# Performance work log

Hardware: AMD Instinct MI355X
Metric: run time of the kernel (lower is better)

The kernel has to match this reference:

```python
import jax, jax.numpy as jnp
import numpy as np

N, C, K, H = 100000, 128, 16, 128
MIX_IN = 2 * C + 1 + C   # x, mean_feat, boundary_score, coord_embed
GATE_IN = 2 * C + 1


def _mlp2(x, w1, b1, w2, b2):
    # Linear -> GELU(exact) -> Linear (dropout=0 at eval)
    return jax.nn.gelu(x @ w1 + b1, approximate=False) @ w2 + b2


def setup_inputs() -> dict:
    key = jax.random.key(0)
    ks = jax.random.split(key, 16)
    s = 0.02
    return {
        "feats": jax.random.normal(ks[0], (N, C), jnp.float32),
        "points": jax.random.normal(ks[1], (N, 3), jnp.float32),
        "neighbors": jax.random.randint(ks[2], (N, K), 0, N, jnp.int64),
        "ln_g": jnp.ones((C,), jnp.float32),
        "ln_b": jnp.zeros((C,), jnp.float32),
        "cp_w1": jax.random.normal(ks[3], (3, H), jnp.float32) * s,
        "cp_b1": jnp.zeros((H,), jnp.float32),
        "cp_w2": jax.random.normal(ks[4], (H, C), jnp.float32) * s,
        "cp_b2": jnp.zeros((C,), jnp.float32),
        "bd_w1": jax.random.normal(ks[5], (2, H), jnp.float32) * s,
        "bd_b1": jnp.zeros((H,), jnp.float32),
        "bd_w2": jax.random.normal(ks[6], (H, 1), jnp.float32) * s,
        "bd_b2": jnp.zeros((1,), jnp.float32),
        "mix_w1": jax.random.normal(ks[7], (MIX_IN, H), jnp.float32) * s,
        "mix_b1": jnp.zeros((H,), jnp.float32),
        "mix_w2": jax.random.normal(ks[8], (H, C), jnp.float32) * s,
        "mix_b2": jnp.zeros((C,), jnp.float32),
        "gate_w1": jax.random.normal(ks[9], (GATE_IN, H), jnp.float32) * s,
        "gate_b1": jnp.zeros((H,), jnp.float32),
        "gate_w2": jax.random.normal(ks[10], (H, C), jnp.float32) * s,
        "gate_b2": jnp.zeros((C,), jnp.float32),
        "out_w": jax.random.normal(ks[11], (C, C), jnp.float32) * s,
        "out_b": jnp.zeros((C,), jnp.float32),
    }


def _forward(feats, points, neighbors, ln_g, ln_b, cp_w1, cp_b1, cp_w2, cp_b2,
             bd_w1, bd_b1, bd_w2, bd_b2, mix_w1, mix_b1, mix_w2, mix_b2,
             gate_w1, gate_b1, gate_w2, gate_b2, out_w, out_b):
    n = feats.shape[0]
    # LayerNorm (eps=1e-5, torch default)
    mu = feats.mean(-1, keepdims=True)
    var = jnp.mean((feats - mu) ** 2, -1, keepdims=True)
    x = (feats - mu) * jax.lax.rsqrt(var + 1e-5) * ln_g + ln_b

    # sanitize neighbors
    valid = ((neighbors >= 0) & (neighbors < n)).astype(x.dtype)  # [N,K]
    safe = jnp.clip(neighbors, 0, n - 1)

    neigh_feats = x[safe]        # [N,K,C]
    neigh_points = points[safe]  # [N,K,3]
    denom = jnp.maximum(valid.sum(1, keepdims=True), 1.0)  # [N,1]
    w = valid[..., None]
    mean_feat = (neigh_feats * w).sum(1) / denom    # [N,C]
    mean_point = (neigh_points * w).sum(1) / denom  # [N,3]

    feat_diff = jnp.linalg.norm(x - mean_feat, axis=-1, keepdims=True)       # [N,1]
    coord_diff = jnp.linalg.norm(points - mean_point, axis=-1, keepdims=True)

    boundary = jax.nn.sigmoid(_mlp2(jnp.concatenate([feat_diff, coord_diff], -1),
                                    bd_w1, bd_b1, bd_w2, bd_b2))  # [N,1]

    # normalize points globally
    centered = points - points.mean(0, keepdims=True)
    scale = jnp.maximum(jnp.abs(centered).max(0, keepdims=True), 1e-6)
    coord_embed = _mlp2(centered / scale, cp_w1, cp_b1, cp_w2, cp_b2)  # [N,C]

    refined = _mlp2(jnp.concatenate([x, mean_feat, boundary, coord_embed], -1),
                    mix_w1, mix_b1, mix_w2, mix_b2)
    gate = jax.nn.sigmoid(_mlp2(jnp.concatenate([x, mean_feat, boundary], -1),
                                gate_w1, gate_b1, gate_w2, gate_b2))
    refined = (gate * refined) @ out_w + out_b
    return feats + refined


def reference(feats, points, neighbors, ln_g, ln_b, cp_w1, cp_b1, cp_w2, cp_b2,
              bd_w1, bd_b1, bd_w2, bd_b2, mix_w1, mix_b1, mix_w2, mix_b2,
              gate_w1, gate_b1, gate_w2, gate_b2, out_w, out_b):
    return _forward(feats, points, neighbors, ln_g, ln_b, cp_w1, cp_b1, cp_w2, cp_b2,
                    bd_w1, bd_b1, bd_w2, bd_b2, mix_w1, mix_b1, mix_w2, mix_b2,
                    gate_w1, gate_b1, gate_w2, gate_b2, out_w, out_b)
```

## Files before the change

### kernel.cpp

```cpp
#include <hip/hip_runtime.h>
#include <math.h>

constexpr int C    = 128;
constexpr int K    = 16;
constexpr int H    = 128;
constexpr int NB2  = 256;
constexpr int WPTS = 32;
constexpr int PB   = 128;
constexpr int HSU  = 68;

constexpr int WT_MIX   = 0;
constexpr int WT_GATE  = 49152;
constexpr int WT_CP2   = 81920;
constexpr int WT_MIX2  = 98304;
constexpr int WT_GATE2 = 114688;
constexpr int WT_OUT   = 131072;
constexpr int WT_TOTAL = 147456;

typedef __attribute__((ext_vector_type(8))) short short8;
typedef __attribute__((ext_vector_type(4))) short short4v;
typedef __attribute__((ext_vector_type(4))) float f32x4;

__device__ __forceinline__ short f2bf(float f) {
    unsigned u = __float_as_uint(f);
    unsigned r = (u + 0x7fffu + ((u >> 16) & 1u)) >> 16;
    return (short)r;
}
__device__ __forceinline__ float bflo(unsigned v) { return __uint_as_float(v << 16); }
__device__ __forceinline__ float bfhi(unsigned v) { return __uint_as_float(v & 0xffff0000u); }
__device__ __forceinline__ float rcpf(float v) { return __builtin_amdgcn_rcpf(v); }

__device__ __forceinline__ float e5m2f(unsigned b) {
    union { unsigned short u; _Float16 h; } cv;
    cv.u = (unsigned short)((b & 0xFFu) << 8);
    return (float)cv.h;
}
__device__ __forceinline__ unsigned f2e5m2(float x) {
    union { _Float16 h; unsigned short u; } cv;
    cv.h = (_Float16)x;
    return ((unsigned)cv.u + 0x7Fu + ((cv.u >> 8) & 1u)) >> 8;
}

__device__ __forceinline__ float gelu_f(float x) {
    float a = fabsf(x) * 0.70710678118654752440f;
    float t = rcpf(1.0f + 0.3275911f * a);
    float p = t * (0.254829592f + t * (-0.284496736f + t * (1.421413741f
            + t * (-1.453152027f + t * 1.061405429f))));
    float e = __expf(-a * a);
    float er = 1.0f - p * e;
    return 0.5f * x * (1.0f + copysignf(er, x));
}
__device__ __forceinline__ float sigm(float v) { return rcpf(1.0f + __expf(-v)); }

__global__ __launch_bounds__(256) void prep_wt(
    const float* __restrict__ mix_w1, const float* __restrict__ gate_w1,
    const float* __restrict__ cp_w2,  const float* __restrict__ mix_w2,
    const float* __restrict__ gate_w2, const float* __restrict__ out_w,
    const float* __restrict__ points,
    short* __restrict__ wt, unsigned* __restrict__ xb_zero,
    unsigned* __restrict__ xg_zero, float* __restrict__ pts4, int n)
{
    int b = blockIdx.x;
    if (b == 36) {
        if (threadIdx.x < 64) xb_zero[threadIdx.x] = 0u;
        else if (threadIdx.x < 96) xg_zero[threadIdx.x - 64] = 0u;
        return;
    }
    if (b >= 37) {
        int i = (b - 37) * 256 + threadIdx.x;
        if (i < n) {
            pts4[i * 4 + 0] = points[i * 3 + 0];
            pts4[i * 4 + 1] = points[i * 3 + 1];
            pts4[i * 4 + 2] = points[i * 3 + 2];
            pts4[i * 4 + 3] = 0.0f;
        } else if (i == n) {
            pts4[i * 4 + 0] = 0.0f; pts4[i * 4 + 1] = 0.0f;
            pts4[i * 4 + 2] = 0.0f; pts4[i * 4 + 3] = 0.0f;
        }
        return;
    }
    const float* src; int off; int c; bool skip256 = false;
    if (b < 12)      { src = mix_w1;  off = WT_MIX;   c = b;      skip256 = true; }
    else if (b < 20) { src = gate_w1; off = WT_GATE;  c = b - 12; }
    else if (b < 24) { src = cp_w2;   off = WT_CP2;   c = b - 20; }
    else if (b < 28) { src = mix_w2;  off = WT_MIX2;  c = b - 24; }
    else if (b < 32) { src = gate_w2; off = WT_GATE2; c = b - 28; }
    else             { src = out_w;   off = WT_OUT;   c = b - 32; }
    for (int ii = 0; ii < 16; ++ii) {
        int e = ii * 256 + threadIdx.x;
        int j = e & 7, l = (e >> 3) & 63, t = e >> 9;
        int k = c * 32 + ((l >> 4) * 8) + j;
        int nn = t * 16 + (l & 15);
        int kk = (skip256 && k >= 256) ? k + 1 : k;
        wt[off + c * 4096 + e] = f2bf(src[kk * C + nn]);
    }
}

__global__ __launch_bounds__(256) void ln_kernel(
    const float* __restrict__ feats, const float* __restrict__ g,
    const float* __restrict__ b, unsigned* __restrict__ xb,
    unsigned short* __restrict__ xg, int n)
{
    const int lane = threadIdx.x & 63;
    const int wave = threadIdx.x >> 6;
    const int i = blockIdx.x * 4 + wave;
    if (i >= n) return;
    const float2 f = *(const float2*)(feats + i * C + 2 * lane);
    float s = f.x + f.y;
    #pragma unroll
    for (int o = 32; o > 0; o >>= 1) s += __shfl_xor(s, o, 64);
    const float mu = s * (1.0f / C);
    const float d0 = f.x - mu, d1 = f.y - mu;
    float v = d0 * d0 + d1 * d1;
    #pragma unroll
    for (int o = 32; o > 0; o >>= 1) v += __shfl_xor(v, o, 64);
    const float rs = rsqrtf(v * (1.0f / C) + 1e-5f);
    const float x0 = d0 * rs * g[2 * lane] + b[2 * lane];
    const float x1 = d1 * rs * g[2 * lane + 1] + b[2 * lane + 1];
    xb[(size_t)i * 64 + lane] =
        (unsigned)(unsigned short)f2bf(x0) | ((unsigned)(unsigned short)f2bf(x1) << 16);
    xg[(size_t)i * 64 + lane] =
        (unsigned short)(f2e5m2(x0) | (f2e5m2(x1) << 8));
}

__global__ __launch_bounds__(256) void pstat_partial(
    const float* __restrict__ pts, float* __restrict__ partial, int n)
{
    __shared__ float sm[256];
    const int tid = threadIdx.x;
    float s[3] = {0, 0, 0};
    float mn[3] = {1e30f, 1e30f, 1e30f};
    float mx[3] = {-1e30f, -1e30f, -1e30f};
    for (int i = blockIdx.x * blockDim.x + tid; i < n; i += gridDim.x * blockDim.x) {
        #pragma unroll
        for (int c = 0; c < 3; ++c) {
            float v = pts[i * 3 + c];
            s[c] += v; mn[c] = fminf(mn[c], v); mx[c] = fmaxf(mx[c], v);
        }
    }
    for (int q = 0; q < 9; ++q) {
        float v = (q < 3) ? s[q] : (q < 6) ? mn[q - 3] : mx[q - 6];
        sm[tid] = v;
        __syncthreads();
        for (int o = 128; o > 0; o >>= 1) {
            if (tid < o) {
                float a = sm[tid], c = sm[tid + o];
                sm[tid] = (q < 3) ? a + c : (q < 6) ? fminf(a, c) : fmaxf(a, c);
            }
            __syncthreads();
        }
        if (tid == 0) partial[blockIdx.x * 9 + q] = sm[0];
        __syncthreads();
    }
}

__global__ __launch_bounds__(256) void pstat_final(
    const float* __restrict__ partial, float* __restrict__ stats, int n)
{
    __shared__ float sm[256];
    const int tid = threadIdx.x;
    for (int q = 0; q < 9; ++q) {
        float v = partial[tid * 9 + q];
        sm[tid] = v;
        __syncthreads();
        for (int o = 128; o > 0; o >>= 1) {
            if (tid < o) {
                float a = sm[tid], c = sm[tid + o];
                sm[tid] = (q < 3) ? a + c : (q < 6) ? fminf(a, c) : fmaxf(a, c);
            }
            __syncthreads();
        }
        if (tid == 0) sm[q] = sm[0];
        __syncthreads();
    }
    if (tid < 3) {
        float mean = sm[tid] / (float)n;
        float scale = fmaxf(fmaxf(sm[6 + tid] - mean, mean - sm[3 + tid]), 1e-6f);
        stats[tid] = mean;
        stats[3 + tid] = scale;
    }
}

__global__ __launch_bounds__(256, 2) void main_kernel(
    const unsigned* __restrict__ xb, const unsigned* __restrict__ xg,
    const float* __restrict__ pts4, const float* __restrict__ feats,
    const int* __restrict__ neighbors,
    const float* __restrict__ stats, const short* __restrict__ wt,
    const float* __restrict__ cp_w1, const float* __restrict__ cp_b1,
    const float* __restrict__ cp_b2,
    const float* __restrict__ bd_w1, const float* __restrict__ bd_b1,
    const float* __restrict__ bd_w2, const float* __restrict__ bd_b2,
    const float* __restrict__ mix_w1, const float* __restrict__ mix_b1,
    const float* __restrict__ mix_b2,
    const float* __restrict__ gate_w1, const float* __restrict__ gate_b1,
    const float* __restrict__ gate_b2,
    const float* __restrict__ out_b,
    float* __restrict__ out, int n)
{
    __shared__ __align__(16) char lds[73216];
    unsigned* mf_s  = (unsigned*)lds;
    unsigned* hid_s = (unsigned*)(lds + 34816);
    float* denom_s  = (float*)(lds + 69632);
    float* pts_s    = denom_s + 128;
    float* cd_s     = pts_s + 512;
    float* bd_s     = cd_s + 128;

    const int tid  = threadIdx.x;
    const int lane = tid & 63;
    const int w    = tid >> 6;
    const int m16  = lane & 15;
    const int h4   = lane >> 4;
    const int i0   = blockIdx.x * PB;
    const int wv32 = w * WPTS;
    const int i0w  = i0 + wv32;
    int* nb_w = (int*)(hid_s + (size_t)wv32 * HSU);

    {
        const int p0 = lane >> 2;
        const int jb = 4 * (lane & 3);
        const int r0 = min(i0w + p0, n - 1);
        const int r1 = min(i0w + 16 + p0, n - 1);
        const int4 A0 = *(const int4*)(neighbors + (size_t)r0 * K + jb);
        const int4 A1 = *(const int4*)(neighbors + (size_t)r1 * K + jb);

        const int q00 = ((unsigned)A0.x < (unsigned)n) ? A0.x : n;
        const int q01 = ((unsigned)A0.y < (unsigned)n) ? A0.y : n;
        const int q02 = ((unsigned)A0.z < (unsigned)n) ? A0.z : n;
        const int q03 = ((unsigned)A0.w < (unsigned)n) ? A0.w : n;
        const int q10 = ((unsigned)A1.x < (unsigned)n) ? A1.x : n;
        const int q11 = ((unsigned)A1.y < (unsigned)n) ? A1.y : n;
        const int q12 = ((unsigned)A1.z < (unsigned)n) ? A1.z : n;
        const int q13 = ((unsigned)A1.w < (unsigned)n) ? A1.w : n;

        *(int4*)&nb_w[4 * lane]       = make_int4(q00, q01, q02, q03);
        *(int4*)&nb_w[256 + 4 * lane] = make_int4(q10, q11, q12, q13);

        float c0 = (float)((q00 != n) + (q01 != n) + (q02 != n) + (q03 != n));
        float c1 = (float)((q10 != n) + (q11 != n) + (q12 != n) + (q13 != n));
        c0 += __shfl_xor(c0, 1, 64); c0 += __shfl_xor(c0, 2, 64);
        c1 += __shfl_xor(c1, 1, 64); c1 += __shfl_xor(c1, 2, 64);
        const float d0 = fmaxf(c0, 1.0f), d1 = fmaxf(c1, 1.0f);
        if ((lane & 3) == 0) {
            denom_s[wv32 + p0]      = d0;
            denom_s[wv32 + 16 + p0] = d1;
        }

        f32x4 s0 = *(const f32x4*)(pts4 + 4 * q00);
        s0 += *(const f32x4*)(pts4 + 4 * q01);
        s0 += *(const f32x4*)(pts4 + 4 * q02);
        s0 += *(const f32x4*)(pts4 + 4 * q03);
        f32x4 s1 = *(const f32x4*)(pts4 + 4 * q10);
        s1 += *(const f32x4*)(pts4 + 4 * q11);
        s1 += *(const f32x4*)(pts4 + 4 * q12);
        s1 += *(const f32x4*)(pts4 + 4 * q13);
        #pragma unroll
        for (int c = 0; c < 3; ++c) {
            s0[c] += __shfl_xor(s0[c], 1, 64); s0[c] += __shfl_xor(s0[c], 2, 64);
            s1[c] += __shfl_xor(s1[c], 1, 64); s1[c] += __shfl_xor(s1[c], 2, 64);
        }
        if ((lane & 3) == 0) {
            const float rd0 = rcpf(d0), rd1 = rcpf(d1);
            const f32x4 pv0 = *(const f32x4*)(pts4 + 4 * r0);
            const f32x4 pv1 = *(const f32x4*)(pts4 + 4 * r1);
            const float e00 = pv0[0] - s0[0] * rd0, e01 = pv0[1] - s0[1] * rd0, e02 = pv0[2] - s0[2] * rd0;
            const float e10 = pv1[0] - s1[0] * rd1, e11 = pv1[1] - s1[1] * rd1, e12 = pv1[2] - s1[2] * rd1;
            cd_s[wv32 + p0]      = sqrtf(e00 * e00 + e01 * e01 + e02 * e02);
            cd_s[wv32 + 16 + p0] = sqrtf(e10 * e10 + e11 * e11 + e12 * e12);
        }
    }

    if (lane < WPTS) {
        const int ipp = min(i0w + lane, n - 1);
        const f32x4 pv = *(const f32x4*)(pts4 + 4 * ipp);
        pts_s[(wv32 + lane) * 4 + 0] = (pv[0] - stats[0]) * rcpf(stats[3]);
        pts_s[(wv32 + lane) * 4 + 1] = (pv[1] - stats[1]) * rcpf(stats[4]);
        pts_s[(wv32 + lane) * 4 + 2] = (pv[2] - stats[2]) * rcpf(stats[5]);
    }

    {
        const int ul   = lane & 31;
        const int half = lane >> 5;
        float w1f[4], w1c[4], b1v[4], w2v[4];
        #pragma unroll
        for (int j = 0; j < 4; ++j) {
            int u = ul + 32 * j;
            w1f[j] = bd_w1[u]; w1c[j] = bd_w1[H + u];
            b1v[j] = bd_b1[u]; w2v[j] = bd_w2[u];
        }
        const float bb2 = bd_b2[0];

        unsigned cur[16], nxt[16];
        #pragma unroll
        for (int k = 0; k < K; ++k) {
            const int r = nb_w[half * K + k];
            cur[k] = xg[(size_t)r * 32 + ul];
        }
        for (int pr = 0; pr < 16; ++pr) {
            if (pr < 15) {
                #pragma unroll
                for (int k = 0; k < K; ++k) {
                    const int r = nb_w[((pr + 1) * 2 + half) * K + k];
                    nxt[k] = xg[(size_t)r * 32 + ul];
                }
            }
            float f0 = 0, f1 = 0, f2 = 0, f3 = 0;
            #pragma unroll
            for (int k = 0; k < K; ++k) {
                const unsigned u = cur[k];
                f0 += e5m2f(u); f1 += e5m2f(u >> 8);
                f2 += e5m2f(u >> 16); f3 += e5m2f(u >> 24);
            }
            const int p = 2 * pr + half;
            const float rden = rcpf(denom_s[wv32 + p]);
            f0 *= rden; f1 *= rden; f2 *= rden; f3 *= rden;
            short4v pk; pk[0] = f2bf(f0); pk[1] = f2bf(f1); pk[2] = f2bf(f2); pk[3] = f2bf(f3);
            *(short4v*)((short*)mf_s + (size_t)(wv32 + p) * (HSU * 2) + ul * 4) = pk;

            const int ipp = min(i0w + p, n - 1);
            const uint2 xv = *(const uint2*)(xb + (size_t)ipp * 64 + 2 * ul);
            const float d0 = bflo(xv.x) - f0, d1 = bfhi(xv.x) - f1;
            const float d2 = bflo(xv.y) - f2, d3 = bfhi(xv.y) - f3;
            float ss = d0 * d0 + d1 * d1 + d2 * d2 + d3 * d3;
            #pragma unroll
            for (int o = 16; o > 0; o >>= 1) ss += __shfl_xor(ss, o, 64);
            const float fd = sqrtf(ss);
            const float cd = cd_s[wv32 + p];
            float s = 0.0f;
            #pragma unroll
            for (int j = 0; j < 4; ++j)
                s += gelu_f(fd * w1f[j] + cd * w1c[j] + b1v[j]) * w2v[j];
            #pragma unroll
            for (int o = 16; o > 0; o >>= 1) s += __shfl_xor(s, o, 64);
            if (ul == 0) bd_s[wv32 + p] = sigm(s + bb2);
            #pragma unroll
            for (int k = 0; k < K; ++k) cur[k] = nxt[k];
        }
    }

    const int pr0 = wv32 + m16, pr1 = wv32 + 16 + m16;
    const int ig0 = i0 + pr0,   ig1 = i0 + pr1;
    const int ip0 = min(ig0, n - 1), ip1 = min(ig1, n - 1);
    const unsigned* xr0  = xb + (size_t)ip0 * 64;
    const unsigned* xr1  = xb + (size_t)ip1 * 64;
    const unsigned* mfr0 = mf_s + pr0 * HSU;
    const unsigned* mfr1 = mf_s + pr1 * HSU;
    unsigned* hr0 = hid_s + pr0 * HSU;
    unsigned* hr1 = hid_s + pr1 * HSU;

    {
        const float px0 = pts_s[pr0 * 4], py0 = pts_s[pr0 * 4 + 1], pz0 = pts_s[pr0 * 4 + 2];
        const float px1 = pts_s[pr1 * 4], py1 = pts_s[pr1 * 4 + 1], pz1 = pts_s[pr1 * 4 + 2];
        f32x4 a0[8], a1[8];
        #pragma unroll
        for (int t = 0; t < 8; ++t) { a0[t] = (f32x4)0.0f; a1[t] = (f32x4)0.0f; }
        #pragma unroll
        for (int c = 0; c < 4; ++c) {
            short8 af0, af1;
            #pragma unroll
            for (int j = 0; j < 8; ++j) {
                const int hh = c * 32 + h4 * 8 + j;
                const float wa = cp_w1[hh], wb = cp_w1[H + hh], wc2 = cp_w1[2 * H + hh];
                const float bb = cp_b1[hh];
                af0[j] = f2bf(gelu_f(bb + px0 * wa + py0 * wb + pz0 * wc2));
                af1[j] = f2bf(gelu_f(bb + px1 * wa + py1 * wb + pz1 * wc2));
            }
            const short* wcp = wt + WT_CP2 + c * 4096 + lane * 8;
            #pragma unroll
            for (int t = 0; t < 8; ++t) {
                const short8 wf = *(const short8*)(wcp + t * 512);
                a0[t] = __builtin_amdgcn_mfma_f32_16x16x32_bf16(wf, af0, a0[t], 0, 0, 0);
                a1[t] = __builtin_amdgcn_mfma_f32_16x16x32_bf16(wf, af1, a1[t], 0, 0, 0);
            }
        }
        #pragma unroll
        for (int t = 0; t < 8; ++t) {
            const f32x4 bb = *(const f32x4*)(cp_b2 + t * 16 + h4 * 4);
            const f32x4 v0 = a0[t] + bb, v1 = a1[t] + bb;
            short4v pk0, pk1;
            #pragma unroll
            for (int r = 0; r < 4; ++r) { pk0[r] = f2bf(v0[r]); pk1[r] = f2bf(v1[r]); }
            *(short4v*)((short*)hr0 + t * 16 + h4 * 4) = pk0;
            *(short4v*)((short*)hr1 + t * 16 + h4 * 4) = pk1;
        }
    }

    const float bdp0 = bd_s[pr0], bdp1 = bd_s[pr1];

    {
        f32x4 a0[8], a1[8];
        #pragma unroll
        for (int t = 0; t < 8; ++t) { a0[t] = (f32x4)0.0f; a1[t] = (f32x4)0.0f; }
        #pragma unroll
        for (int c = 0; c < 12; ++c) {
            short8 af0, af1;
            if (c < 4) {
                af0 = *(const short8*)(xr0 + c * 16 + h4 * 4);
                af1 = *(const short8*)(xr1 + c * 16 + h4 * 4);
            } else if (c < 8) {
                af0 = *(const short8*)(mfr0 + (c - 4) * 16 + h4 * 4);
                af1 = *(const short8*)(mfr1 + (c - 4) * 16 + h4 * 4);
            } else {
                af0 = *(const short8*)(hr0 + (c - 8) * 16 + h4 * 4);
                af1 = *(const short8*)(hr1 + (c - 8) * 16 + h4 * 4);
            }
            const short* wmc = wt + WT_MIX + c * 4096 + lane * 8;
            #pragma unroll
            for (int t = 0; t < 8; ++t) {
                const short8 wf = *(const short8*)(wmc + t * 512);
                a0[t] = __builtin_amdgcn_mfma_f32_16x16x32_bf16(wf, af0, a0[t], 0, 0, 0);
                a1[t] = __builtin_amdgcn_mfma_f32_16x16x32_bf16(wf, af1, a1[t], 0, 0, 0);
            }
        }
        #pragma unroll
        for (int t = 0; t < 8; ++t) {
            const int col = t * 16 + h4 * 4;
            const f32x4 wb = *(const f32x4*)(mix_w1 + 256 * C + col);
            const f32x4 bb = *(const f32x4*)(mix_b1 + col);
            const f32x4 v0 = a0[t] + bdp0 * wb + bb;
            const f32x4 v1 = a1[t] + bdp1 * wb + bb;
            short4v pk0, pk1;
            #pragma unroll
            for (int r = 0; r < 4; ++r) { pk0[r] = f2bf(gelu_f(v0[r])); pk1[r] = f2bf(gelu_f(v1[r])); }
            *(short4v*)((short*)hr0 + col) = pk0;
            *(short4v*)((short*)hr1 + col) = pk1;
        }
    }

    f32x4 rf0[8], rf1[8];
    {
        #pragma unroll
        for (int t = 0; t < 8; ++t) { rf0[t] = (f32x4)0.0f; rf1[t] = (f32x4)0.0f; }
        #pragma unroll
        for (int c = 0; c < 4; ++c) {
            const short8 af0 = *(const short8*)(hr0 + c * 16 + h4 * 4);
            const short8 af1 = *(const short8*)(hr1 + c * 16 + h4 * 4);
            const short* wmc = wt + WT_MIX2 + c * 4096 + lane * 8;
            #pragma unroll
            for (int t = 0; t < 8; ++t) {
                const short8 wf = *(const short8*)(wmc + t * 512);
                rf0[t] = __builtin_amdgcn_mfma_f32_16x16x32_bf16(wf, af0, rf0[t], 0, 0, 0);
                rf1[t] = __builtin_amdgcn_mfma_f32_16x16x32_bf16(wf, af1, rf1[t], 0, 0, 0);
            }
        }
        #pragma unroll
        for (int t = 0; t < 8; ++t) {
            const f32x4 bb = *(const f32x4*)(mix_b2 + t * 16 + h4 * 4);
            rf0[t] += bb; rf1[t] += bb;
        }
    }

    {
        f32x4 a0[8], a1[8];
        #pragma unroll
        for (int t = 0; t < 8; ++t) { a0[t] = (f32x4)0.0f; a1[t] = (f32x4)0.0f; }
        #pragma unroll
        for (int c = 0; c < 8; ++c) {
            short8 af0, af1;
            if (c < 4) {
                af0 = *(const short8*)(xr0 + c * 16 + h4 * 4);
                af1 = *(const short8*)(xr1 + c * 16 + h4 * 4);
            } else {
                af0 = *(const short8*)(mfr0 + (c - 4) * 16 + h4 * 4);
                af1 = *(const short8*)(mfr1 + (c - 4) * 16 + h4 * 4);
            }
            const short* wgc = wt + WT_GATE + c * 4096 + lane * 8;
            #pragma unroll
            for (int t = 0; t < 8; ++t) {
                const short8 wf = *(const short8*)(wgc + t * 512);
                a0[t] = __builtin_amdgcn_mfma_f32_16x16x32_bf16(wf, af0, a0[t], 0, 0, 0);
                a1[t] = __builtin_amdgcn_mfma_f32_16x16x32_bf16(wf, af1, a1[t], 0, 0, 0);
            }
        }
        #pragma unroll
        for (int t = 0; t < 8; ++t) {
            const int col = t * 16 + h4 * 4;
            const f32x4 wb = *(const f32x4*)(gate_w1 + 256 * C + col);
            const f32x4 bb = *(const f32x4*)(gate_b1 + col);
            const f32x4 v0 = a0[t] + bdp0 * wb + bb;
            const f32x4 v1 = a1[t] + bdp1 * wb + bb;
            short4v pk0, pk1;
            #pragma unroll
            for (int r = 0; r < 4; ++r) { pk0[r] = f2bf(gelu_f(v0[r])); pk1[r] = f2bf(gelu_f(v1[r])); }
            *(short4v*)((short*)hr0 + col) = pk0;
            *(short4v*)((short*)hr1 + col) = pk1;
        }
    }

    {
        f32x4 a0[8], a1[8];
        #pragma unroll
        for (int t = 0; t < 8; ++t) { a0[t] = (f32x4)0.0f; a1[t] = (f32x4)0.0f; }
        #pragma unroll
        for (int c = 0; c < 4; ++c) {
            const short8 af0 = *(const short8*)(hr0 + c * 16 + h4 * 4);
            const short8 af1 = *(const short8*)(hr1 + c * 16 + h4 * 4);
            const short* wgc = wt + WT_GATE2 + c * 4096 + lane * 8;
            #pragma unroll
            for (int t = 0; t < 8; ++t) {
                const short8 wf = *(const short8*)(wgc + t * 512);
                a0[t] = __builtin_amdgcn_mfma_f32_16x16x32_bf16(wf, af0, a0[t], 0, 0, 0);
                a1[t] = __builtin_amdgcn_mfma_f32_16x16x32_bf16(wf, af1, a1[t], 0, 0, 0);
            }
        }
        #pragma unroll
        for (int t = 0; t < 8; ++t) {
            const int col = t * 16 + h4 * 4;
            const f32x4 bb = *(const f32x4*)(gate_b2 + col);
            short4v pk0, pk1;
            #pragma unroll
            for (int r = 0; r < 4; ++r) {
                pk0[r] = f2bf(sigm(a0[t][r] + bb[r]) * rf0[t][r]);
                pk1[r] = f2bf(sigm(a1[t][r] + bb[r]) * rf1[t][r]);
            }
            *(short4v*)((short*)hr0 + col) = pk0;
            *(short4v*)((short*)hr1 + col) = pk1;
        }
    }

    {
        f32x4 a0[8], a1[8];
        #pragma unroll
        for (int t = 0; t < 8; ++t) { a0[t] = (f32x4)0.0f; a1[t] = (f32x4)0.0f; }
        #pragma unroll
        for (int c = 0; c < 4; ++c) {
            const short8 af0 = *(const short8*)(hr0 + c * 16 + h4 * 4);
            const short8 af1 = *(const short8*)(hr1 + c * 16 + h4 * 4);
            const short* woc = wt + WT_OUT + c * 4096 + lane * 8;
            #pragma unroll
            for (int t = 0; t < 8; ++t) {
                const short8 wf = *(const short8*)(woc + t * 512);
                a0[t] = __builtin_amdgcn_mfma_f32_16x16x32_bf16(wf, af0, a0[t], 0, 0, 0);
                a1[t] = __builtin_amdgcn_mfma_f32_16x16x32_bf16(wf, af1, a1[t], 0, 0, 0);
            }
        }
        #pragma unroll
        for (int t = 0; t < 8; ++t) {
            const int col = t * 16 + h4 * 4;
            const f32x4 bb = *(const f32x4*)(out_b + col);
            const f32x4 fv0 = *(const f32x4*)(feats + (size_t)ip0 * C + col);
            const f32x4 fv1 = *(const f32x4*)(feats + (size_t)ip1 * C + col);
            const f32x4 v0 = a0[t] + bb + fv0;
            const f32x4 v1 = a1[t] + bb + fv1;
            if (ig0 < n) *(f32x4*)(out + (size_t)ig0 * C + col) = v0;
            if (ig1 < n) *(f32x4*)(out + (size_t)ig1 * C + col) = v1;
        }
    }
}

extern "C" void kernel_launch(void* const* d_in, const int* in_sizes, int n_in,
                              void* d_out, int out_size, void* d_ws, size_t ws_size,
                              hipStream_t stream)
{
    const float* feats     = (const float*)d_in[0];
    const float* points    = (const float*)d_in[1];
    const int*   neighbors = (const int*)d_in[2];
    const float* ln_g      = (const float*)d_in[3];
    const float* ln_b      = (const float*)d_in[4];
    const float* cp_w1     = (const float*)d_in[5];
    const float* cp_b1     = (const float*)d_in[6];
    const float* cp_w2     = (const float*)d_in[7];
    const float* cp_b2     = (const float*)d_in[8];
    const float* bd_w1     = (const float*)d_in[9];
    const float* bd_b1     = (const float*)d_in[10];
    const float* bd_w2     = (const float*)d_in[11];
    const float* bd_b2     = (const float*)d_in[12];
    const float* mix_w1    = (const float*)d_in[13];
    const float* mix_b1    = (const float*)d_in[14];
    const float* mix_w2    = (const float*)d_in[15];
    const float* mix_b2    = (const float*)d_in[16];
    const float* gate_w1   = (const float*)d_in[17];
    const float* gate_b1   = (const float*)d_in[18];
    const float* gate_w2   = (const float*)d_in[19];
    const float* gate_b2   = (const float*)d_in[20];
    const float* out_w     = (const float*)d_in[21];
    const float* out_b     = (const float*)d_in[22];
    float* out = (float*)d_out;
    (void)n_in; (void)out_size; (void)ws_size;

    const int n = in_sizes[0] / C;

    char* base = (char*)d_ws;
    unsigned* xb        = (unsigned*)base;
    unsigned short* xg  = (unsigned short*)(base + (size_t)(n + 1) * 256);
    float* pts4         = (float*)(base + (size_t)(n + 1) * 256 + (size_t)(n + 1) * 128);
    short* wt           = (short*)((char*)pts4 + (size_t)(n + 1) * 16);
    float* partial      = (float*)((char*)wt + (size_t)WT_TOTAL * 2);
    float* stats        = partial + NB2 * 9;

    const int prep_blocks = 37 + (n + 256) / 256;
    prep_wt<<<prep_blocks, 256, 0, stream>>>(
        mix_w1, gate_w1, cp_w2, mix_w2, gate_w2, out_w, points,
        wt, xb + (size_t)n * 64, (unsigned*)(xg + (size_t)n * 64), pts4, n);
    ln_kernel<<<(n + 3) / 4, 256, 0, stream>>>(feats, ln_g, ln_b, xb, xg, n);
    pstat_partial<<<NB2, 256, 0, stream>>>(points, partial, n);
    pstat_final<<<1, 256, 0, stream>>>(partial, stats, n);
    main_kernel<<<(n + PB - 1) / PB, 256, 0, stream>>>(
        xb, (const unsigned*)xg, pts4, feats, neighbors, stats, wt,
        cp_w1, cp_b1, cp_b2, bd_w1, bd_b1, bd_w2, bd_b2,
        mix_w1, mix_b1, mix_b2, gate_w1, gate_b1, gate_b2,
        out_b, out, n);
}
```

Baseline: 340.0 us.

## Split main kernel into gather and GEMM kernels and merge prep launches

The monolithic main kernel becomes two kernels. A gather kernel runs at higher occupancy, computes the neighbor-mean features and the boundary score, and writes them to global memory. A GEMM kernel then runs the MLP chain and reorders it so the gate MLP goes first, keeping the gate in packed bf16 registers instead of holding the fp32 mix accumulators. The prep, layernorm and point-stat partial kernels are merged into one launch, and the e5m2 neighbor sum now uses packed half adds. This trades an extra global round trip for mean features against better latency hiding and smaller LDS and register footprints, at some precision risk from fp16 accumulation and a bf16-rounded gate.

Result: slower. 401.2 us (+18.0%).

```diff
diff --git a/kernel.cpp b/kernel.cpp
--- a/kernel.cpp
+++ b/kernel.cpp
@@ -20,6 +20,7 @@
 typedef __attribute__((ext_vector_type(8))) short short8;
 typedef __attribute__((ext_vector_type(4))) short short4v;
 typedef __attribute__((ext_vector_type(4))) float f32x4;
+typedef _Float16 h2 __attribute__((ext_vector_type(2)));
 
 __device__ __forceinline__ short f2bf(float f) {
     unsigned u = __float_as_uint(f);
@@ -28,13 +29,11 @@
 }
 __device__ __forceinline__ float bflo(unsigned v) { return __uint_as_float(v << 16); }
 __device__ __forceinline__ float bfhi(unsigned v) { return __uint_as_float(v & 0xffff0000u); }
+__device__ __forceinline__ float bf2f(short s) {
+    return __uint_as_float(((unsigned)(unsigned short)s) << 16);
+}
 __device__ __forceinline__ float rcpf(float v) { return __builtin_amdgcn_rcpf(v); }
 
-__device__ __forceinline__ float e5m2f(unsigned b) {
-    union { unsigned short u; _Float16 h; } cv;
-    cv.u = (unsigned short)((b & 0xFFu) << 8);
-    return (float)cv.h;
-}
 __device__ __forceinline__ unsigned f2e5m2(float x) {
     union { _Float16 h; unsigned short u; } cv;
     cv.h = (_Float16)x;
@@ -52,22 +51,45 @@
 }
 __device__ __forceinline__ float sigm(float v) { return rcpf(1.0f + __expf(-v)); }
 
-__global__ __launch_bounds__(256) void prep_wt(
+__global__ __launch_bounds__(256) void prep_all(
     const float* __restrict__ mix_w1, const float* __restrict__ gate_w1,
     const float* __restrict__ cp_w2,  const float* __restrict__ mix_w2,
     const float* __restrict__ gate_w2, const float* __restrict__ out_w,
-    const float* __restrict__ points,
-    short* __restrict__ wt, unsigned* __restrict__ xb_zero,
-    unsigned* __restrict__ xg_zero, float* __restrict__ pts4, int n)
+    const float* __restrict__ points, const float* __restrict__ feats,
+    const float* __restrict__ ln_g, const float* __restrict__ ln_b,
+    short* __restrict__ wt, unsigned* __restrict__ xb,
+    unsigned short* __restrict__ xg, float* __restrict__ pts4,
+    float* __restrict__ partial, int n, int np4)
 {
-    int b = blockIdx.x;
+    __shared__ float sm[256];
+    const int b   = blockIdx.x;
+    const int tid = threadIdx.x;
+
+    if (b < 36) {
+        const float* src; int off; int c; bool skip256 = false;
+        if (b < 12)      { src = mix_w1;  off = WT_MIX;   c = b;      skip256 = true; }
+        else if (b < 20) { src = gate_w1; off = WT_GATE;  c = b - 12; }
+        else if (b < 24) { src = cp_w2;   off = WT_CP2;   c = b - 20; }
+        else if (b < 28) { src = mix_w2;  off = WT_MIX2;  c = b - 24; }
+        else if (b < 32) { src = gate_w2; off = WT_GATE2; c = b - 28; }
+        else             { src = out_w;   off = WT_OUT;   c = b - 32; }
+        for (int ii = 0; ii < 16; ++ii) {
+            int e = ii * 256 + tid;
+            int j = e & 7, l = (e >> 3) & 63, t = e >> 9;
+            int k = c * 32 + ((l >> 4) * 8) + j;
+            int nn = t * 16 + (l & 15);
+            int kk = (skip256 && k >= 256) ? k + 1 : k;
+            wt[off + c * 4096 + e] = f2bf(src[kk * C + nn]);
+        }
+        return;
+    }
     if (b == 36) {
-        if (threadIdx.x < 64) xb_zero[threadIdx.x] = 0u;
-        else if (threadIdx.x < 96) xg_zero[threadIdx.x - 64] = 0u;
+        if (tid < 64) xb[(size_t)n * 64 + tid] = 0u;
+        else if (tid < 96) ((unsigned*)xg)[(size_t)n * 32 + (tid - 64)] = 0u;
         return;
     }
-    if (b >= 37) {
-        int i = (b - 37) * 256 + threadIdx.x;
+    if (b < 37 + np4) {
+        int i = (b - 37) * 256 + tid;
         if (i < n) {
             pts4[i * 4 + 0] = points[i * 3 + 0];
             pts4[i * 4 + 1] = points[i * 3 + 1];
@@ -79,31 +101,38 @@
         }
         return;
     }
-    const float* src; int off; int c; bool skip256 = false;
-    if (b < 12)      { src = mix_w1;  off = WT_MIX;   c = b;      skip256 = true; }
-    else if (b < 20) { src = gate_w1; off = WT_GATE;  c = b - 12; }
-    else if (b < 24) { src = cp_w2;   off = WT_CP2;   c = b - 20; }
-    else if (b < 28) { src = mix_w2;  off = WT_MIX2;  c = b - 24; }
-    else if (b < 32) { src = gate_w2; off = WT_GATE2; c = b - 28; }
-    else             { src = out_w;   off = WT_OUT;   c = b - 32; }
-    for (int ii = 0; ii < 16; ++ii) {
-        int e = ii * 256 + threadIdx.x;
-        int j = e & 7, l = (e >> 3) & 63, t = e >> 9;
-        int k = c * 32 + ((l >> 4) * 8) + j;
-        int nn = t * 16 + (l & 15);
-        int kk = (skip256 && k >= 256) ? k + 1 : k;
-        wt[off + c * 4096 + e] = f2bf(src[kk * C + nn]);
-    }
-}
-
-__global__ __launch_bounds__(256) void ln_kernel(
-    const float* __restrict__ feats, const float* __restrict__ g,
-    const float* __restrict__ b, unsigned* __restrict__ xb,
-    unsigned short* __restrict__ xg, int n)
-{
-    const int lane = threadIdx.x & 63;
-    const int wave = threadIdx.x >> 6;
-    const int i = blockIdx.x * 4 + wave;
+    if (b < 37 + np4 + NB2) {
+        const int bb = b - 37 - np4;
+        float s[3] = {0, 0, 0};
+        float mn[3] = {1e30f, 1e30f, 1e30f};
+        float mx[3] = {-1e30f, -1e30f, -1e30f};
+        for (int i = bb * 256 + tid; i < n; i += NB2 * 256) {
+            #pragma unroll
+            for (int c = 0; c < 3; ++c) {
+                float v = points[i * 3 + c];
+                s[c] += v; mn[c] = fminf(mn[c], v); mx[c] = fmaxf(mx[c], v);
+            }
+        }
+        for (int q = 0; q < 9; ++q) {
+            float v = (q < 3) ? s[q] : (q < 6) ? mn[q - 3] : mx[q - 6];
+            sm[tid] = v;
+            __syncthreads();
+            for (int o = 128; o > 0; o >>= 1) {
+                if (tid < o) {
+                    float a = sm[tid], c = sm[tid + o];
+                    sm[tid] = (q < 3) ? a + c : (q < 6) ? fminf(a, c) : fmaxf(a, c);
+                }
+                __syncthreads();
+            }
+            if (tid == 0) partial[bb * 9 + q] = sm[0];
+            __syncthreads();
+        }
+        return;
+    }
+
+    const int lane = tid & 63;
+    const int wave = tid >> 6;
+    const int i = (b - 37 - np4 - NB2) * 4 + wave;
     if (i >= n) return;
     const float2 f = *(const float2*)(feats + i * C + 2 * lane);
     float s = f.x + f.y;
@@ -115,43 +144,12 @@
     #pragma unroll
     for (int o = 32; o > 0; o >>= 1) v += __shfl_xor(v, o, 64);
     const float rs = rsqrtf(v * (1.0f / C) + 1e-5f);
-    const float x0 = d0 * rs * g[2 * lane] + b[2 * lane];
-    const float x1 = d1 * rs * g[2 * lane + 1] + b[2 * lane + 1];
+    const float x0 = d0 * rs * ln_g[2 * lane] + ln_b[2 * lane];
+    const float x1 = d1 * rs * ln_g[2 * lane + 1] + ln_b[2 * lane + 1];
     xb[(size_t)i * 64 + lane] =
         (unsigned)(unsigned short)f2bf(x0) | ((unsigned)(unsigned short)f2bf(x1) << 16);
     xg[(size_t)i * 64 + lane] =
         (unsigned short)(f2e5m2(x0) | (f2e5m2(x1) << 8));
-}
-
-__global__ __launch_bounds__(256) void pstat_partial(
-    const float* __restrict__ pts, float* __restrict__ partial, int n)
-{
-    __shared__ float sm[256];
-    const int tid = threadIdx.x;
-    float s[3] = {0, 0, 0};
-    float mn[3] = {1e30f, 1e30f, 1e30f};
-    float mx[3] = {-1e30f, -1e30f, -1e30f};
-    for (int i = blockIdx.x * blockDim.x + tid; i < n; i += gridDim.x * blockDim.x) {
-        #pragma unroll
-        for (int c = 0; c < 3; ++c) {
-            float v = pts[i * 3 + c];
-            s[c] += v; mn[c] = fminf(mn[c], v); mx[c] = fmaxf(mx[c], v);
-        }
-    }
-    for (int q = 0; q < 9; ++q) {
-        float v = (q < 3) ? s[q] : (q < 6) ? mn[q - 3] : mx[q - 6];
-        sm[tid] = v;
-        __syncthreads();
-        for (int o = 128; o > 0; o >>= 1) {
-            if (tid < o) {
-                float a = sm[tid], c = sm[tid + o];
-                sm[tid] = (q < 3) ? a + c : (q < 6) ? fminf(a, c) : fmaxf(a, c);
-            }
-            __syncthreads();
-        }
-        if (tid == 0) partial[blockIdx.x * 9 + q] = sm[0];
-        __syncthreads();
-    }
 }
 
 __global__ __launch_bounds__(256) void pstat_final(
@@ -181,39 +179,24 @@
     }
 }
 
-__global__ __launch_bounds__(256, 2) void main_kernel(
+__global__ __launch_bounds__(256, 4) void gather_kernel(
     const unsigned* __restrict__ xb, const unsigned* __restrict__ xg,
-    const float* __restrict__ pts4, const float* __restrict__ feats,
-    const int* __restrict__ neighbors,
-    const float* __restrict__ stats, const short* __restrict__ wt,
-    const float* __restrict__ cp_w1, const float* __restrict__ cp_b1,
-    const float* __restrict__ cp_b2,
+    const float* __restrict__ pts4, const int* __restrict__ neighbors,
     const float* __restrict__ bd_w1, const float* __restrict__ bd_b1,
     const float* __restrict__ bd_w2, const float* __restrict__ bd_b2,
-    const float* __restrict__ mix_w1, const float* __restrict__ mix_b1,
-    const float* __restrict__ mix_b2,
-    const float* __restrict__ gate_w1, const float* __restrict__ gate_b1,
-    const float* __restrict__ gate_b2,
-    const float* __restrict__ out_b,
-    float* __restrict__ out, int n)
+    unsigned* __restrict__ mf_g, float* __restrict__ bd_g, int n)
 {
-    __shared__ __align__(16) char lds[73216];
-    unsigned* mf_s  = (unsigned*)lds;
-    unsigned* hid_s = (unsigned*)(lds + 34816);
-    float* denom_s  = (float*)(lds + 69632);
-    float* pts_s    = denom_s + 128;
-    float* cd_s     = pts_s + 512;
-    float* bd_s     = cd_s + 128;
+    __shared__ int   nb_s[4][512];
+    __shared__ float denom_s[128];
+    __shared__ float cd_s[128];
 
     const int tid  = threadIdx.x;
     const int lane = tid & 63;
     const int w    = tid >> 6;
-    const int m16  = lane & 15;
-    const int h4   = lane >> 4;
     const int i0   = blockIdx.x * PB;
     const int wv32 = w * WPTS;
     const int i0w  = i0 + wv32;
-    int* nb_w = (int*)(hid_s + (size_t)wv32 * HSU);
+    int* nb_w = nb_s[w];
 
     {
         const int p0 = lane >> 2;
@@ -269,14 +252,6 @@
         }
     }
 
-    if (lane < WPTS) {
-        const int ipp = min(i0w + lane, n - 1);
-        const f32x4 pv = *(const f32x4*)(pts4 + 4 * ipp);
-        pts_s[(wv32 + lane) * 4 + 0] = (pv[0] - stats[0]) * rcpf(stats[3]);
-        pts_s[(wv32 + lane) * 4 + 1] = (pv[1] - stats[1]) * rcpf(stats[4]);
-        pts_s[(wv32 + lane) * 4 + 2] = (pv[2] - stats[2]) * rcpf(stats[5]);
-    }
-
     {
         const int ul   = lane & 31;
         const int half = lane >> 5;
@@ -303,18 +278,26 @@
                     nxt[k] = xg[(size_t)r * 32 + ul];
                 }
             }
-            float f0 = 0, f1 = 0, f2 = 0, f3 = 0;
+            union UH { unsigned u; h2 h; };
+            UH a02, a13; a02.u = 0u; a13.u = 0u;
             #pragma unroll
             for (int k = 0; k < K; ++k) {
                 const unsigned u = cur[k];
-                f0 += e5m2f(u); f1 += e5m2f(u >> 8);
-                f2 += e5m2f(u >> 16); f3 += e5m2f(u >> 24);
-            }
+                UH lo, hi;
+                lo.u = (u << 8) & 0xFF00FF00u;
+                hi.u = u & 0xFF00FF00u;
+                a02.h += lo.h;
+                a13.h += hi.h;
+            }
+            float f0 = (float)a02.h[0], f2 = (float)a02.h[1];
+            float f1 = (float)a13.h[0], f3 = (float)a13.h[1];
+
             const int p = 2 * pr + half;
             const float rden = rcpf(denom_s[wv32 + p]);
             f0 *= rden; f1 *= rden; f2 *= rden; f3 *= rden;
             short4v pk; pk[0] = f2bf(f0); pk[1] = f2bf(f1); pk[2] = f2bf(f2); pk[3] = f2bf(f3);
-            *(short4v*)((short*)mf_s + (size_t)(wv32 + p) * (HSU * 2) + ul * 4) = pk;
+            if (i0w + p < n)
+                *(short4v*)((short*)mf_g + (size_t)(i0w + p) * 128 + ul * 4) = pk;
 
             const int ipp = min(i0w + p, n - 1);
             const uint2 xv = *(const uint2*)(xb + (size_t)ipp * 64 + 2 * ul);
@@ -331,25 +314,122 @@
                 s += gelu_f(fd * w1f[j] + cd * w1c[j] + b1v[j]) * w2v[j];
             #pragma unroll
             for (int o = 16; o > 0; o >>= 1) s += __shfl_xor(s, o, 64);
-            if (ul == 0) bd_s[wv32 + p] = sigm(s + bb2);
+            if (ul == 0 && i0w + p < n) bd_g[i0w + p] = sigm(s + bb2);
             #pragma unroll
             for (int k = 0; k < K; ++k) cur[k] = nxt[k];
         }
     }
+}
+
+__global__ __launch_bounds__(256, 3) void gemm_kernel(
+    const unsigned* __restrict__ xb, const unsigned* __restrict__ mf_g,
+    const float* __restrict__ bd_g, const float* __restrict__ pts4,
+    const float* __restrict__ feats, const float* __restrict__ stats,
+    const short* __restrict__ wt,
+    const float* __restrict__ cp_w1, const float* __restrict__ cp_b1,
+    const float* __restrict__ cp_b2,
+    const float* __restrict__ mix_w1, const float* __restrict__ mix_b1,
+    const float* __restrict__ mix_b2,
+    const float* __restrict__ gate_w1, const float* __restrict__ gate_b1,
+    const float* __restrict__ gate_b2,
+    const float* __restrict__ out_b, float* __restrict__ out, int n)
+{
+    __shared__ __align__(16) unsigned hid_s[128 * HSU];
+
+    const int tid  = threadIdx.x;
+    const int lane = tid & 63;
+    const int w    = tid >> 6;
+    const int m16  = lane & 15;
+    const int h4   = lane >> 4;
+    const int i0   = blockIdx.x * PB;
+    const int wv32 = w * WPTS;
 
     const int pr0 = wv32 + m16, pr1 = wv32 + 16 + m16;
     const int ig0 = i0 + pr0,   ig1 = i0 + pr1;
     const int ip0 = min(ig0, n - 1), ip1 = min(ig1, n - 1);
     const unsigned* xr0  = xb + (size_t)ip0 * 64;
     const unsigned* xr1  = xb + (size_t)ip1 * 64;
-    const unsigned* mfr0 = mf_s + pr0 * HSU;
-    const unsigned* mfr1 = mf_s + pr1 * HSU;
+    const unsigned* mfr0 = mf_g + (size_t)ip0 * 64;
+    const unsigned* mfr1 = mf_g + (size_t)ip1 * 64;
     unsigned* hr0 = hid_s + pr0 * HSU;
     unsigned* hr1 = hid_s + pr1 * HSU;
 
-    {
-        const float px0 = pts_s[pr0 * 4], py0 = pts_s[pr0 * 4 + 1], pz0 = pts_s[pr0 * 4 + 2];
-        const float px1 = pts_s[pr1 * 4], py1 = pts_s[pr1 * 4 + 1], pz1 = pts_s[pr1 * 4 + 2];
+    const float bdp0 = bd_g[ip0], bdp1 = bd_g[ip1];
+
+    {
+        f32x4 a0[8], a1[8];
+        #pragma unroll
+        for (int t = 0; t < 8; ++t) { a0[t] = (f32x4)0.0f; a1[t] = (f32x4)0.0f; }
+        #pragma unroll
+        for (int c = 0; c < 8; ++c) {
+            short8 af0, af1;
+            if (c < 4) {
+                af0 = *(const short8*)(xr0 + c * 16 + h4 * 4);
+                af1 = *(const short8*)(xr1 + c * 16 + h4 * 4);
+            } else {
+                af0 = *(const short8*)(mfr0 + (c - 4) * 16 + h4 * 4);
+                af1 = *(const short8*)(mfr1 + (c - 4) * 16 + h4 * 4);
+            }
+            const short* wgc = wt + WT_GATE + c * 4096 + lane * 8;
+            #pragma unroll
+            for (int t = 0; t < 8; ++t) {
+                const short8 wf = *(const short8*)(wgc + t * 512);
+                a0[t] = __builtin_amdgcn_mfma_f32_16x16x32_bf16(wf, af0, a0[t], 0, 0, 0);
+                a1[t] = __builtin_amdgcn_mfma_f32_16x16x32_bf16(wf, af1, a1[t], 0, 0, 0);
+            }
+        }
+        #pragma unroll
+        for (int t = 0; t < 8; ++t) {
+            const int col = t * 16 + h4 * 4;
+            const f32x4 wb = *(const f32x4*)(gate_w1 + 256 * C + col);
+            const f32x4 bb = *(const f32x4*)(gate_b1 + col);
+            const f32x4 v0 = a0[t] + bdp0 * wb + bb;
+            const f32x4 v1 = a1[t] + bdp1 * wb + bb;
+            short4v pk0, pk1;
+            #pragma unroll
+            for (int r = 0; r < 4; ++r) { pk0[r] = f2bf(gelu_f(v0[r])); pk1[r] = f2bf(gelu_f(v1[r])); }
+            *(short4v*)((short*)hr0 + col) = pk0;
+            *(short4v*)((short*)hr1 + col) = pk1;
+        }
+    }
+
+    short4v gpk0[8], gpk1[8];
+    {
+        f32x4 a0[8], a1[8];
+        #pragma unroll
+        for (int t = 0; t < 8; ++t) { a0[t] = (f32x4)0.0f; a1[t] = (f32x4)0.0f; }
+        #pragma unroll
+        for (int c = 0; c < 4; ++c) {
+            const short8 af0 = *(const short8*)(hr0 + c * 16 + h4 * 4);
+            const short8 af1 = *(const short8*)(hr1 + c * 16 + h4 * 4);
+            const short* wgc = wt + WT_GATE2 + c * 4096 + lane * 8;
+            #pragma unroll
+            for (int t = 0; t < 8; ++t) {
+                const short8 wf = *(const short8*)(wgc + t * 512);
+                a0[t] = __builtin_amdgcn_mfma_f32_16x16x32_bf16(wf, af0, a0[t], 0, 0, 0);
+                a1[t] = __builtin_amdgcn_mfma_f32_16x16x32_bf16(wf, af1, a1[t], 0, 0, 0);
+            }
+        }
+        #pragma unroll
+        for (int t = 0; t < 8; ++t) {
+            const f32x4 bb = *(const f32x4*)(gate_b2 + t * 16 + h4 * 4);
+            #pragma unroll
+            for (int r = 0; r < 4; ++r) {
+                gpk0[t][r] = f2bf(sigm(a0[t][r] + bb[r]));
+                gpk1[t][r] = f2bf(sigm(a1[t][r] + bb[r]));
+            }
+        }
+    }
+
+    {
+        const f32x4 pv0 = *(const f32x4*)(pts4 + 4 * ip0);
+        const f32x4 pv1 = *(const f32x4*)(pts4 + 4 * ip1);
+        const float px0 = (pv0[0] - stats[0]) * rcpf(stats[3]);
+        const float py0 = (pv0[1] - stats[1]) * rcpf(stats[4]);
+        const float pz0 = (pv0[2] - stats[2]) * rcpf(stats[5]);
+        const float px1 = (pv1[0] - stats[0]) * rcpf(stats[3]);
+        const float py1 = (pv1[1] - stats[1]) * rcpf(stats[4]);
+        const float pz1 = (pv1[2] - stats[2]) * rcpf(stats[5]);
         f32x4 a0[8], a1[8];
         #pragma unroll
         for (int t = 0; t < 8; ++t) { a0[t] = (f32x4)0.0f; a1[t] = (f32x4)0.0f; }
@@ -383,8 +463,6 @@
             *(short4v*)((short*)hr1 + t * 16 + h4 * 4) = pk1;
         }
     }
-
-    const float bdp0 = bd_s[pr0], bdp1 = bd_s[pr1];
 
     {
         f32x4 a0[8], a1[8];
@@ -426,10 +504,10 @@
         }
     }
 
-    f32x4 rf0[8], rf1[8];
-    {
-        #pragma unroll
-        for (int t = 0; t < 8; ++t) { rf0[t] = (f32x4)0.0f; rf1[t] = (f32x4)0.0f; }
+    {
+        f32x4 a0[8], a1[8];
+        #pragma unroll
+        for (int t = 0; t < 8; ++t) { a0[t] = (f32x4)0.0f; a1[t] = (f32x4)0.0f; }
         #pragma unroll
         for (int c = 0; c < 4; ++c) {
             const short8 af0 = *(const short8*)(hr0 + c * 16 + h4 * 4);
@@ -438,35 +516,6 @@
             #pragma unroll
             for (int t = 0; t < 8; ++t) {
                 const short8 wf = *(const short8*)(wmc + t * 512);
-                rf0[t] = __builtin_amdgcn_mfma_f32_16x16x32_bf16(wf, af0, rf0[t], 0, 0, 0);
-                rf1[t] = __builtin_amdgcn_mfma_f32_16x16x32_bf16(wf, af1, rf1[t], 0, 0, 0);
-            }
-        }
-        #pragma unroll
-        for (int t = 0; t < 8; ++t) {
-            const f32x4 bb = *(const f32x4*)(mix_b2 + t * 16 + h4 * 4);
-            rf0[t] += bb; rf1[t] += bb;
-        }
-    }
-
-    {
-        f32x4 a0[8], a1[8];
-        #pragma unroll
-        for (int t = 0; t < 8; ++t) { a0[t] = (f32x4)0.0f; a1[t] = (f32x4)0.0f; }
-        #pragma unroll
-        for (int c = 0; c < 8; ++c) {
-            short8 af0, af1;
-            if (c < 4) {
-                af0 = *(const short8*)(xr0 + c * 16 + h4 * 4);
-                af1 = *(const short8*)(xr1 + c * 16 + h4 * 4);
-            } else {
-                af0 = *(const short8*)(mfr0 + (c - 4) * 16 + h4 * 4);
-                af1 = *(const short8*)(mfr1 + (c - 4) * 16 + h4 * 4);
-            }
-            const short* wgc = wt + WT_GATE + c * 4096 + lane * 8;
-            #pragma unroll
-            for (int t = 0; t < 8; ++t) {
-                const short8 wf = *(const short8*)(wgc + t * 512);
                 a0[t] = __builtin_amdgcn_mfma_f32_16x16x32_bf16(wf, af0, a0[t], 0, 0, 0);
                 a1[t] = __builtin_amdgcn_mfma_f32_16x16x32_bf16(wf, af1, a1[t], 0, 0, 0);
             }
@@ -474,43 +523,13 @@
         #pragma unroll
         for (int t = 0; t < 8; ++t) {
             const int col = t * 16 + h4 * 4;
-            const f32x4 wb = *(const f32x4*)(gate_w1 + 256 * C + col);
-            const f32x4 bb = *(const f32x4*)(gate_b1 + col);
-            const f32x4 v0 = a0[t] + bdp0 * wb + bb;
-            const f32x4 v1 = a1[t] + bdp1 * wb + bb;
+            const f32x4 bb = *(const f32x4*)(mix_b2 + col);
+            const f32x4 v0 = a0[t] + bb, v1 = a1[t] + bb;
             short4v pk0, pk1;
             #pragma unroll
-            for (int r = 0; r < 4; ++r) { pk0[r] = f2bf(gelu_f(v0[r])); pk1[r] = f2bf(gelu_f(v1[r])); }
-            *(short4v*)((short*)hr0 + col) = pk0;
-            *(short4v*)((short*)hr1 + col) = pk1;
-        }
-    }
-
-    {
-        f32x4 a0[8], a1[8];
-        #pragma unroll
-        for (int t = 0; t < 8; ++t) { a0[t] = (f32x4)0.0f; a1[t] = (f32x4)0.0f; }
-        #pragma unroll
-        for (int c = 0; c < 4; ++c) {
-            const short8 af0 = *(const short8*)(hr0 + c * 16 + h4 * 4);
-            const short8 af1 = *(const short8*)(hr1 + c * 16 + h4 * 4);
-            const short* wgc = wt + WT_GATE2 + c * 4096 + lane * 8;
-            #pragma unroll
-            for (int t = 0; t < 8; ++t) {
-                const short8 wf = *(const short8*)(wgc + t * 512);
-                a0[t] = __builtin_amdgcn_mfma_f32_16x16x32_bf16(wf, af0, a0[t], 0, 0, 0);
-                a1[t] = __builtin_amdgcn_mfma_f32_16x16x32_bf16(wf, af1, a1[t], 0, 0, 0);
-            }
-        }
-        #pragma unroll
-        for (int t = 0; t < 8; ++t) {
-            const int col = t * 16 + h4 * 4;
-            const f32x4 bb = *(const f32x4*)(gate_b2 + col);
-            short4v pk0, pk1;
-            #pragma unroll
             for (int r = 0; r < 4; ++r) {
-                pk0[r] = f2bf(sigm(a0[t][r] + bb[r]) * rf0[t][r]);
-                pk1[r] = f2bf(sigm(a1[t][r] + bb[r]) * rf1[t][r]);
+                pk0[r] = f2bf(bf2f(gpk0[t][r]) * v0[r]);
+                pk1[r] = f2bf(bf2f(gpk1[t][r]) * v1[r]);
             }
             *(short4v*)((short*)hr0 + col) = pk0;
             *(short4v*)((short*)hr1 + col) = pk1;
@@ -582,21 +601,27 @@
     char* base = (char*)d_ws;
     unsigned* xb        = (unsigned*)base;
     unsigned short* xg  = (unsigned short*)(base + (size_t)(n + 1) * 256);
-    float* pts4         = (float*)(base + (size_t)(n + 1) * 256 + (size_t)(n + 1) * 128);
+    float* pts4         = (float*)(base + (size_t)(n + 1) * 384);
     short* wt           = (short*)((char*)pts4 + (size_t)(n + 1) * 16);
     float* partial      = (float*)((char*)wt + (size_t)WT_TOTAL * 2);
     float* stats        = partial + NB2 * 9;
-
-    const int prep_blocks = 37 + (n + 256) / 256;
-    prep_wt<<<prep_blocks, 256, 0, stream>>>(
-        mix_w1, gate_w1, cp_w2, mix_w2, gate_w2, out_w, points,
-        wt, xb + (size_t)n * 64, (unsigned*)(xg + (size_t)n * 64), pts4, n);
-    ln_kernel<<<(n + 3) / 4, 256, 0, stream>>>(feats, ln_g, ln_b, xb, xg, n);
-    pstat_partial<<<NB2, 256, 0, stream>>>(points, partial, n);
+    unsigned* mf_g      = (unsigned*)((char*)stats + 32);
+    float* bd_g         = (float*)((char*)mf_g + (size_t)n * 256);
+
+    const int np4 = (n + 256) / 256;
+    const int nln = (n + 3) / 4;
+    const int nb_main = (n + PB - 1) / PB;
+
+    prep_all<<<37 + np4 + NB2 + nln, 256, 0, stream>>>(
+        mix_w1, gate_w1, cp_w2, mix_w2, gate_w2, out_w,
+        points, feats, ln_g, ln_b,
+        wt, xb, xg, pts4, partial, n, np4);
     pstat_final<<<1, 256, 0, stream>>>(partial, stats, n);
-    main_kernel<<<(n + PB - 1) / PB, 256, 0, stream>>>(
-        xb, (const unsigned*)xg, pts4, feats, neighbors, stats, wt,
-        cp_w1, cp_b1, cp_b2, bd_w1, bd_b1, bd_w2, bd_b2,
-        mix_w1, mix_b1, mix_b2, gate_w1, gate_b1, gate_b2,
-        out_b, out, n);
-}
+    gather_kernel<<<nb_main, 256, 0, stream>>>(
+        xb, (const unsigned*)xg, pts4, neighbors,
+        bd_w1, bd_b1, bd_w2, bd_b2, mf_g, bd_g, n);
+    gemm_kernel<<<nb_main, 256, 0, stream>>>(
+        xb, mf_g, bd_g, pts4, feats, stats, wt,
+        cp_w1, cp_b1, cp_b2, mix_w1, mix_b1, mix_b2,
+        gate_w1, gate_b1, gate_b2, out_b, out, n);
+}
```
